# Performance work log

Measured on AMD Instinct MI355X. Metric: run time of the kernel, lower is better.

Reference implementation:

```python
import jax, jax.numpy as jnp
import numpy as np

INTERVAL = 8
HEADS = 4
DIM = 64


def grid_shuffle(x, I):
    # rearrange 'b c (h i) (w j) -> (b i j) c h w' : stride-I residue grouping
    B, C, H, W = x.shape
    h, w = H // I, W // I
    x = x.reshape(B, C, h, I, w, I).transpose(0, 3, 5, 1, 2, 4)
    return x.reshape(B * I * I, C, h, w)


def grid_unshuffle(x, I, B):
    Bp, C, h, w = x.shape
    x = x.reshape(B, I, I, C, h, w).transpose(0, 3, 4, 1, 5, 2)
    return x.reshape(B, C, h * I, w * I)


def conv1x1(x, w, b):
    return jnp.einsum('oc,bchw->bohw', w, x) + b[None, :, None, None]


def pos_bias(h, w, W1, b1, W2, b2):
    # dynamic RPE: MLP over normalized relative coordinates -> [heads, N, N]
    ch = jnp.arange(h)
    cw = jnp.arange(w)
    coords = jnp.stack(jnp.meshgrid(ch, cw, indexing='ij'), -1).reshape(-1, 2).astype(jnp.float32)
    denom = jnp.array([max(h - 1, 1), max(w - 1, 1)], dtype=jnp.float32)
    rel = (coords[:, None, :] - coords[None, :, :]) / denom  # [N,N,2]
    hid = jax.nn.relu(rel @ W1 + b1)
    bias = hid @ W2 + b2  # [N,N,heads]
    return bias.transpose(2, 0, 1)


def mask_attn(q2d, k2d, v2d, bias, pw, pb, heads, scale):
    Bp, C, h, w = q2d.shape
    N, d = h * w, C // heads

    def to_tok(t):  # [Bp,C,h,w] -> [Bp,heads,N,d]
        return t.reshape(Bp, heads, d, N).transpose(0, 1, 3, 2)

    q, k, v = to_tok(q2d), to_tok(k2d), to_tok(v2d)
    attn = jnp.einsum('bhnd,bhmd->bhnm', q * scale, k) + bias[None]
    attn = jax.nn.softmax(attn, axis=-1)
    out = jnp.einsum('bhnm,bhmd->bhnd', attn, v)
    out2d = out.transpose(0, 1, 3, 2).reshape(Bp, C, h, w)
    return conv1x1(out2d, pw, pb)


def setup_inputs() -> dict:
    key = jax.random.key(0)
    ks = jax.random.split(key, 14)
    pos_hidden = DIM // 4  # 16
    s = 0.02
    return {
        'x': jax.random.normal(ks[0], (2, DIM, 160, 160), jnp.float32),
        'qkv_w': jax.random.normal(ks[1], (3 * DIM, DIM), jnp.float32) * s,
        'qkv_b': jnp.zeros((3 * DIM,), jnp.float32),
        'grid_w': jax.random.normal(ks[2], (DIM, DIM), jnp.float32) * s,
        'grid_b': jnp.zeros((DIM,), jnp.float32),
        'pos_w1': jax.random.normal(ks[3], (2, pos_hidden), jnp.float32) * s,
        'pos_b1': jnp.zeros((pos_hidden,), jnp.float32),
        'pos_w2': jax.random.normal(ks[4], (pos_hidden, HEADS), jnp.float32) * s,
        'pos_b2': jnp.zeros((HEADS,), jnp.float32),
        'proj1_w': jax.random.normal(ks[5], (DIM, DIM), jnp.float32) * s,
        'proj1_b': jnp.zeros((DIM,), jnp.float32),
        'proj2_w': jax.random.normal(ks[6], (DIM, DIM), jnp.float32) * s,
        'proj2_b': jnp.zeros((DIM,), jnp.float32),
    }


def reference(x, qkv_w, qkv_b, grid_w, grid_b, pos_w1, pos_b1, pos_w2, pos_b2,
              proj1_w, proj1_b, proj2_w, proj2_b):
    I = INTERVAL
    scale = (DIM // HEADS) ** -0.5
    B, C, H, W = x.shape
    qkv = conv1x1(x, qkv_w, qkv_b)
    x_grid = conv1x1(grid_shuffle(x, I), grid_w, grid_b)
    qkv = grid_shuffle(qkv, I)
    bias = pos_bias(H // I, W // I, pos_w1, pos_b1, pos_w2, pos_b2)
    q, k, v = jnp.split(qkv, 3, axis=1)
    out = mask_attn(x_grid, k, v, bias, proj1_w, proj1_b, HEADS, scale)
    out = mask_attn(q, x_grid, out, bias, proj2_w, proj2_b, HEADS, scale)
    return grid_unshuffle(out, I, B)
```

## Files before the change

kernel.cpp:

```cpp
#include <hip/hip_runtime.h>
#include <hip/hip_bf16.h>


#define N_TOK 400
#define NP    416
#define BP    128

typedef short bf16x8 __attribute__((ext_vector_type(8)));
typedef float f32x16 __attribute__((ext_vector_type(16)));

__device__ inline ushort f2bf(float f) {
    __hip_bfloat16 h = __float2bfloat16(f);
    return *reinterpret_cast<ushort*>(&h);
}
__device__ inline float bf2f(ushort u) {
    union { uint i; float f; } v; v.i = (uint)u << 16; return v.f;
}
__device__ inline uint pk2(float a, float b) {
    return (uint)f2bf(a) | ((uint)f2bf(b) << 16);
}
__device__ inline bf16x8 ld16(const ushort* p) {
    union { uint4 q; bf16x8 v; } u;
    u.q = *reinterpret_cast<const uint4*>(p);
    return u.v;
}
__device__ inline float fast_exp2(float x) {
#if __has_builtin(__builtin_amdgcn_exp2f)
    return __builtin_amdgcn_exp2f(x);
#else
    return __expf(x * 0.6931471805599453f);
#endif
}
__device__ inline float fast_rcp(float x) {
#if __has_builtin(__builtin_amdgcn_rcpf)
    return __builtin_amdgcn_rcpf(x);
#else
    return 1.0f / x;
#endif
}

#define L2E 1.4426950408889634f
#define QK_PRESCALE 0.36067376022224085f

__global__ __launch_bounds__(256) void k_prep(
    const float* __restrict__ W1, const float* __restrict__ B1,
    const float* __restrict__ W2, const float* __restrict__ B2,
    const float* __restrict__ qkv_w, const float* __restrict__ qkv_b,
    const float* __restrict__ grid_w, const float* __restrict__ grid_b,
    const float* __restrict__ p1w, const float* __restrict__ p2w,
    float* __restrict__ biasF, ushort* __restrict__ Wc, float* __restrict__ Bc,
    ushort* __restrict__ Wp1, ushort* __restrict__ Wp2)
{
    int blk = blockIdx.x;
    if (blk < 2704) {
        int idx = blk * 256 + threadIdx.x;
        if (idx >= 692224) return;
        int r = idx & 15, lane = (idx >> 4) & 63;
        int tile = idx >> 10;
        int mt = tile % 13, rem = tile / 13, qt = rem % 13, h = rem / 13;
        int n = qt * 32 + (lane & 31);
        int m = mt * 32 + (r & 3) + 8 * (r >> 2) + 4 * (lane >> 5);
        float val = 0.0f;
        if (n < 400 && m < 400) {
            float r0 = (float)(n / 20 - m / 20) * (1.0f / 19.0f);
            float r1 = (float)(n % 20 - m % 20) * (1.0f / 19.0f);
            float o = B2[h];
#pragma unroll
            for (int k = 0; k < 16; ++k) {
                float hh = r0 * W1[k] + r1 * W1[16 + k] + B1[k];
                hh = fmaxf(hh, 0.0f);
                o += hh * W2[k * 4 + h];
            }
            val = o * L2E;
        }
        biasF[idx] = val;
    } else {
        int t = (blk - 2704) * 256 + threadIdx.x;
        if (t < 16384) {
            int oc = t >> 6, k = t & 63;
            float v = (oc < 192) ? qkv_w[oc * 64 + k] : grid_w[(oc - 192) * 64 + k];
            Wc[t] = f2bf(v);
        } else if (t < 16384 + 4096) {
            Wp1[t - 16384] = f2bf(p1w[t - 16384]);
        } else if (t < 16384 + 8192) {
            Wp2[t - 16384 - 4096] = f2bf(p2w[t - 16384 - 4096]);
        } else if (t < 16384 + 8192 + 256) {
            int oc = t - 16384 - 8192;
            Bc[oc] = (oc < 192) ? qkv_b[oc] : grid_b[oc - 192];
        }
    }
}

__global__ __launch_bounds__(256) void k_conv(
    const float* __restrict__ x, const ushort* __restrict__ Wc,
    const float* __restrict__ Bc,
    ushort* __restrict__ Qb, ushort* __restrict__ Kb,
    ushort* __restrict__ Vb, ushort* __restrict__ XGb)
{
    __shared__ __align__(16) ushort XL[32 * 64];
    int blk = blockIdx.x;
    int b = blk / 800, rem = blk % 800;
    int H0 = rem / 5, wt = rem % 5;
    int w0 = wt * 32;
    int tid = threadIdx.x;

    {
        int c = tid >> 2, q4 = tid & 3;
        const float* xr = x + ((size_t)(b * 64 + c) * 160 + H0) * 160 + w0 + q4 * 8;
        float4 f0 = *reinterpret_cast<const float4*>(xr);
        float4 f1 = *reinterpret_cast<const float4*>(xr + 4);
        char* base = reinterpret_cast<char*>(XL);
#pragma unroll
        for (int k = 0; k < 8; ++k) {
            float v = (k < 4) ? ((const float*)&f0)[k] : ((const float*)&f1)[k - 4];
            int p = q4 * 8 + k;
            int byt = p * 128 + ((2 * c) ^ ((p & 7) << 4));
            *reinterpret_cast<ushort*>(base + byt) = f2bf(v);
        }
    }

    int lane = tid & 63, w = tid >> 6;
    int l31 = lane & 31, hi = lane >> 5;

    bf16x8 wf[2][4];
#pragma unroll
    for (int nt = 0; nt < 2; ++nt)
#pragma unroll
        for (int kk = 0; kk < 4; ++kk)
            wf[nt][kk] = ld16(&Wc[(size_t)(w * 64 + nt * 32 + l31) * 64 + kk * 16 + hi * 8]);
    __syncthreads();

    f32x16 acc0 = 0.0f, acc1 = 0.0f;
    const char* base = reinterpret_cast<const char*>(XL);
#pragma unroll
    for (int kk = 0; kk < 4; ++kk) {
        int byt = l31 * 128 + (((kk * 32 + hi * 16)) ^ ((l31 & 7) << 4));
        bf16x8 xf;
        {
            union { uint4 q; bf16x8 v; } u;
            u.q = *reinterpret_cast<const uint4*>(base + byt);
            xf = u.v;
        }
        acc0 = __builtin_amdgcn_mfma_f32_32x32x16_bf16(wf[0][kk], xf, acc0, 0, 0, 0);
        acc1 = __builtin_amdgcn_mfma_f32_32x32x16_bf16(wf[1][kk], xf, acc1, 0, 0, 0);
    }

    int W0 = w0 + l31, ww = W0 >> 3, j = W0 & 7;
    int bp = b * 64 + (H0 & 7) * 8 + j;
    int n  = (H0 >> 3) * 20 + ww;
    ushort* outb = (w == 0) ? Qb : (w == 1) ? Kb : (w == 2) ? Vb : XGb;
    float mul = (w <= 1) ? QK_PRESCALE : 1.0f;
    ushort* dst = outb + ((size_t)bp * NP + n) * 64;
#pragma unroll
    for (int nt = 0; nt < 2; ++nt) {
        const f32x16& a = nt ? acc1 : acc0;
#pragma unroll
        for (int g = 0; g < 4; ++g) {
            int cc = nt * 32 + 8 * g + 4 * hi;
            int oc = w * 64 + cc;
            uint2 uu;
            uu.x = pk2((a[4 * g + 0] + Bc[oc + 0]) * mul, (a[4 * g + 1] + Bc[oc + 1]) * mul);
            uu.y = pk2((a[4 * g + 2] + Bc[oc + 2]) * mul, (a[4 * g + 3] + Bc[oc + 3]) * mul);
            *reinterpret_cast<uint2*>(dst + cc) = uu;
        }
    }
}

__global__ __launch_bounds__(512, 4) void k_attn_mfma(
    const ushort* __restrict__ Qg, const ushort* __restrict__ Kg,
    const ushort* __restrict__ Vg, const float* __restrict__ biasF,
    ushort* __restrict__ O)
{
    __shared__ ushort Ks[NP * 16];
    __shared__ ushort Vt[16 * 424];
    int blk = blockIdx.x;
    int bp = blk >> 2, h = blk & 3;
    int tid = threadIdx.x;

    const ushort* Ksrc = Kg + (size_t)bp * NP * 64 + h * 16;
#pragma unroll
    for (int it = 0; it < 2; ++it) {
        int i = tid + it * 512;
        if (i < NP * 2) {
            int row = i >> 1, half = i & 1;
            *reinterpret_cast<uint4*>(&Ks[row * 16 + half * 8]) =
                *reinterpret_cast<const uint4*>(&Ksrc[(size_t)row * 64 + half * 8]);
        }
    }
    const ushort* Vsrc = Vg + (size_t)bp * NP * 64 + h * 16;
#pragma unroll
    for (int it = 0; it < 2; ++it) {
        int i = tid + it * 512;
        if (i < 800) {
            int row = i >> 1, hf = i & 1;
            uint4 v = *reinterpret_cast<const uint4*>(&Vsrc[(size_t)row * 64 + hf * 8]);
            const ushort* pv = reinterpret_cast<const ushort*>(&v);
#pragma unroll
            for (int k = 0; k < 8; ++k)
                Vt[(hf * 8 + k) * 424 + row] = pv[k];
        }
    }
    __syncthreads();

    int lane = tid & 63, w = tid >> 6;
    int l31 = lane & 31, hi = lane >> 5;

    for (int qt = w; qt < 13; qt += 8) {
        int qbase = qt * 32;
        bf16x8 qf = ld16(&Qg[((size_t)bp * NP + qbase + l31) * 64 + h * 16 + hi * 8]);
        f32x16 acc = 0.0f;
        const float* bfr = biasF + ((size_t)(h * 169 + qt * 13)) * 1024 + lane * 16;

        float4 cb0 = *reinterpret_cast<const float4*>(bfr + 0);
        float4 cb1 = *reinterpret_cast<const float4*>(bfr + 4);
        float4 cb2 = *reinterpret_cast<const float4*>(bfr + 8);
        float4 cb3 = *reinterpret_cast<const float4*>(bfr + 12);

#pragma unroll
        for (int mt = 0; mt < 13; ++mt) {
            const int mbase = mt * 32;
            float4 nb0, nb1, nb2, nb3;
            if (mt < 12) {
                const float4* nx = reinterpret_cast<const float4*>(bfr + (size_t)(mt + 1) * 1024);
                nb0 = nx[0]; nb1 = nx[1]; nb2 = nx[2]; nb3 = nx[3];
            }

            bf16x8 kf = ld16(&Ks[(mbase + l31) * 16 + hi * 8]);
            f32x16 cin;
            cin[0] = cb0.x; cin[1] = cb0.y; cin[2]  = cb0.z; cin[3]  = cb0.w;
            cin[4] = cb1.x; cin[5] = cb1.y; cin[6]  = cb1.z; cin[7]  = cb1.w;
            cin[8] = cb2.x; cin[9] = cb2.y; cin[10] = cb2.z; cin[11] = cb2.w;
            cin[12] = cb3.x; cin[13] = cb3.y; cin[14] = cb3.z; cin[15] = cb3.w;
            f32x16 sv = __builtin_amdgcn_mfma_f32_32x32x16_bf16(kf, qf, cin, 0, 0, 0);

            const int nv = (mt == 12) ? 8 : 16;
            float p[16];
#pragma unroll
            for (int r = 0; r < 16; ++r)
                if (r < nv) p[r] = fast_exp2(sv[r]);

            {
                uint c4 = pk2(p[0], p[1]), c5 = pk2(p[2], p[3]);
                uint c6 = pk2(p[4], p[5]), c7 = pk2(p[6], p[7]);
                asm("v_permlane32_swap_b32 %0, %1" : "+v"(c4), "+v"(c6));
                asm("v_permlane32_swap_b32 %0, %1" : "+v"(c5), "+v"(c7));
                union { uint u[4]; bf16x8 v; } A;
                A.u[0] = c4; A.u[1] = c5; A.u[2] = c6; A.u[3] = c7;
                bf16x8 vf;
                if (l31 < 16) vf = ld16(&Vt[l31 * 424 + mbase + hi * 8]);
                else { union { uint u[4]; bf16x8 v; } o; o.u[0]=o.u[1]=o.u[2]=o.u[3]=0x3F803F80u; vf = o.v; }
                acc = __builtin_amdgcn_mfma_f32_32x32x16_bf16(A.v, vf, acc, 0, 0, 0);
            }
            if (mt < 12) {
                uint c4 = pk2(p[8], p[9]),  c5 = pk2(p[10], p[11]);
                uint c6 = pk2(p[12], p[13]), c7 = pk2(p[14], p[15]);
                asm("v_permlane32_swap_b32 %0, %1" : "+v"(c4), "+v"(c6));
                asm("v_permlane32_swap_b32 %0, %1" : "+v"(c5), "+v"(c7));
                union { uint u[4]; bf16x8 v; } A;
                A.u[0] = c4; A.u[1] = c5; A.u[2] = c6; A.u[3] = c7;
                bf16x8 vf;
                if (l31 < 16) vf = ld16(&Vt[l31 * 424 + mbase + 16 + hi * 8]);
                else { union { uint u[4]; bf16x8 v; } o; o.u[0]=o.u[1]=o.u[2]=o.u[3]=0x3F803F80u; vf = o.v; }
                acc = __builtin_amdgcn_mfma_f32_32x32x16_bf16(A.v, vf, acc, 0, 0, 0);
            }
            cb0 = nb0; cb1 = nb1; cb2 = nb2; cb3 = nb3;
        }

#pragma unroll
        for (int r = 0; r < 16; ++r) {
            int moff = (r & 3) + 8 * (r >> 2) + 4 * hi;
            int q = qbase + moff;
            float s = __shfl(acc[r], lane | 16);
            if (l31 < 16 && q < N_TOK)
                O[((size_t)bp * 400 + q) * 64 + h * 16 + l31] = f2bf(acc[r] * fast_rcp(s));
        }
    }
}

template<int MODE>
__global__ __launch_bounds__(256) void k_proj(
    const ushort* __restrict__ In, const ushort* __restrict__ Wp,
    const float* __restrict__ Bv, ushort* __restrict__ Out)
{
    __shared__ __align__(16) ushort XL[128 * 64];
    size_t t0 = (size_t)blockIdx.x * 128;
    int tid = threadIdx.x;

    char* basec = reinterpret_cast<char*>(XL);
#pragma unroll
    for (int it = 0; it < 4; ++it) {
        int idx = tid + it * 256;
        int p = idx >> 3, c8 = idx & 7;
        uint4 v = *reinterpret_cast<const uint4*>(In + (t0 + p) * 64 + c8 * 8);
        int byt = p * 128 + ((c8 * 16) ^ ((p & 7) << 4));
        *reinterpret_cast<uint4*>(basec + byt) = v;
    }

    int lane = tid & 63, w = tid >> 6;
    int l31 = lane & 31, hi = lane >> 5;

    bf16x8 wf[2][4];
#pragma unroll
    for (int nt = 0; nt < 2; ++nt)
#pragma unroll
        for (int kk = 0; kk < 4; ++kk)
            wf[nt][kk] = ld16(&Wp[(size_t)(nt * 32 + l31) * 64 + kk * 16 + hi * 8]);
    __syncthreads();

    int prow = w * 32 + l31;
    f32x16 acc0 = 0.0f, acc1 = 0.0f;
#pragma unroll
    for (int kk = 0; kk < 4; ++kk) {
        int byt = prow * 128 + (((kk * 32 + hi * 16)) ^ ((prow & 7) << 4));
        union { uint4 q; bf16x8 v; } u;
        u.q = *reinterpret_cast<const uint4*>(basec + byt);
        acc0 = __builtin_amdgcn_mfma_f32_32x32x16_bf16(wf[0][kk], u.v, acc0, 0, 0, 0);
        acc1 = __builtin_amdgcn_mfma_f32_32x32x16_bf16(wf[1][kk], u.v, acc1, 0, 0, 0);
    }

    size_t t = t0 + prow;
    ushort* dst;
    if (MODE == 0) {
        int bp = (int)(t / 400), n = (int)(t % 400);
        dst = Out + ((size_t)bp * NP + n) * 64;
    } else {
        dst = Out + t * 64;
    }
#pragma unroll
    for (int nt = 0; nt < 2; ++nt) {
        const f32x16& a = nt ? acc1 : acc0;
#pragma unroll
        for (int g = 0; g < 4; ++g) {
            int cc = nt * 32 + 8 * g + 4 * hi;
            uint2 uu;
            uu.x = pk2(a[4 * g + 0] + Bv[cc + 0], a[4 * g + 1] + Bv[cc + 1]);
            uu.y = pk2(a[4 * g + 2] + Bv[cc + 2], a[4 * g + 3] + Bv[cc + 3]);
            *reinterpret_cast<uint2*>(dst + cc) = uu;
        }
    }
}

__global__ __launch_bounds__(256) void k_unshuffle(
    const ushort* __restrict__ In, float* __restrict__ out)
{
    __shared__ __align__(16) ushort il[160 * 64];
    int blk = blockIdx.x;
    int b = blk / 160, rem = blk % 160, iI = rem / 20, hh = rem % 20;
    int tid = threadIdx.x;

    for (int idx = tid; idx < 1280; idx += 256) {
        int j = idx / 160, r2 = idx % 160, ww = r2 / 8, c8 = r2 % 8;
        int bp = b * 64 + iI * 8 + j;
        int n  = hh * 20 + ww;
        uint4 v = reinterpret_cast<const uint4*>(In + ((size_t)bp * 400 + n) * 64)[c8];
        reinterpret_cast<uint4*>(&il[(ww * 8 + j) * 64])[c8] = v;
    }
    __syncthreads();

    int c = tid >> 2, q = tid & 3;
    int H0 = hh * 8 + iI;
    float* og = out + ((size_t)(b * 64 + c) * 160 + H0) * 160;
#pragma unroll
    for (int k = 0; k < 10; ++k) {
        int f = q + 4 * k;
        float4 v;
        v.x = bf2f(il[(4 * f + 0) * 64 + c]);
        v.y = bf2f(il[(4 * f + 1) * 64 + c]);
        v.z = bf2f(il[(4 * f + 2) * 64 + c]);
        v.w = bf2f(il[(4 * f + 3) * 64 + c]);
        reinterpret_cast<float4*>(og)[f] = v;
    }
}

extern "C" void kernel_launch(void* const* d_in, const int* in_sizes, int n_in,
                              void* d_out, int out_size, void* d_ws, size_t ws_size,
                              hipStream_t stream)
{
    const float* x      = (const float*)d_in[0];
    const float* qkv_w  = (const float*)d_in[1];
    const float* qkv_b  = (const float*)d_in[2];
    const float* grid_w = (const float*)d_in[3];
    const float* grid_b = (const float*)d_in[4];
    const float* pw1    = (const float*)d_in[5];
    const float* pb1    = (const float*)d_in[6];
    const float* pw2    = (const float*)d_in[7];
    const float* pb2    = (const float*)d_in[8];
    const float* p1w    = (const float*)d_in[9];
    const float* p1b    = (const float*)d_in[10];
    const float* p2w    = (const float*)d_in[11];
    const float* p2b    = (const float*)d_in[12];

    char* W = (char*)d_ws;
    float*  biasF = (float*)(W + 0);
    ushort* Wc    = (ushort*)(W + 2768896);
    ushort* Wp1   = (ushort*)(W + 2801664);
    ushort* Wp2   = (ushort*)(W + 2809856);
    float*  Bc    = (float*) (W + 2818048);
    const size_t BASE2 = 2819072;
    const size_t BB = (size_t)BP * NP * 64 * 2;
    ushort* Qb = (ushort*)(W + BASE2);
    ushort* Kb = (ushort*)(W + BASE2 + 1 * BB);
    ushort* Vb = (ushort*)(W + BASE2 + 2 * BB);
    ushort* XG = (ushort*)(W + BASE2 + 3 * BB);
    ushort* P1 = (ushort*)(W + BASE2 + 4 * BB);
    const size_t OB = (size_t)BP * 400 * 64 * 2;
    ushort* O1 = (ushort*)(W + BASE2 + 5 * BB);
    ushort* O2 = (ushort*)(W + BASE2 + 5 * BB + OB);
    ushort* OFb = O1;
    float*  out = (float*)d_out;

    k_prep<<<2801, 256, 0, stream>>>(pw1, pb1, pw2, pb2, qkv_w, qkv_b, grid_w, grid_b,
                                     p1w, p2w, biasF, Wc, Bc, Wp1, Wp2);
    k_conv<<<1600, 256, 0, stream>>>(x, Wc, Bc, Qb, Kb, Vb, XG);
    k_attn_mfma<<<512, 512, 0, stream>>>(XG, Kb, Vb, biasF, O1);
    k_proj<0><<<400, 256, 0, stream>>>(O1, Wp1, p1b, P1);
    k_attn_mfma<<<512, 512, 0, stream>>>(Qb, XG, P1, biasF, O2);
    k_proj<1><<<400, 256, 0, stream>>>(O2, Wp2, p2b, OFb);
    k_unshuffle<<<320, 256, 0, stream>>>(OFb, out);
}
```

Measured before the change: 116.0 us.

## Split attention query tiles across two blocks per head for balanced waves

Each (batch, head) attention block is split into two blocks handling 7 and 6 query tiles, so every wave processes at most one tile instead of some waves doing two. The grid doubles to 1024 blocks and unused waves exit early. This removes the per-block tail where a few waves do double work, at the cost of loading K and V into shared memory twice per head. The bias load is also simplified to a single 16-float vector load.

```diff
diff --git a/kernel.cpp b/kernel.cpp
--- a/kernel.cpp
+++ b/kernel.cpp
@@ -174,7 +174,9 @@
     __shared__ ushort Ks[NP * 16];
     __shared__ ushort Vt[16 * 424];
     int blk = blockIdx.x;
-    int bp = blk >> 2, h = blk & 3;
+    int bp = blk >> 3, h = (blk >> 1) & 3, sub = blk & 1;
+    int qt0 = sub ? 7 : 0;
+    int cnt = sub ? 6 : 7;
     int tid = threadIdx.x;
 
     const ushort* Ksrc = Kg + (size_t)bp * NP * 64 + h * 16;
@@ -205,75 +207,65 @@
     int lane = tid & 63, w = tid >> 6;
     int l31 = lane & 31, hi = lane >> 5;
 
-    for (int qt = w; qt < 13; qt += 8) {
-        int qbase = qt * 32;
-        bf16x8 qf = ld16(&Qg[((size_t)bp * NP + qbase + l31) * 64 + h * 16 + hi * 8]);
-        f32x16 acc = 0.0f;
-        const float* bfr = biasF + ((size_t)(h * 169 + qt * 13)) * 1024 + lane * 16;
-
-        float4 cb0 = *reinterpret_cast<const float4*>(bfr + 0);
-        float4 cb1 = *reinterpret_cast<const float4*>(bfr + 4);
-        float4 cb2 = *reinterpret_cast<const float4*>(bfr + 8);
-        float4 cb3 = *reinterpret_cast<const float4*>(bfr + 12);
-
-#pragma unroll
-        for (int mt = 0; mt < 13; ++mt) {
-            const int mbase = mt * 32;
-            float4 nb0, nb1, nb2, nb3;
-            if (mt < 12) {
-                const float4* nx = reinterpret_cast<const float4*>(bfr + (size_t)(mt + 1) * 1024);
-                nb0 = nx[0]; nb1 = nx[1]; nb2 = nx[2]; nb3 = nx[3];
-            }
-
-            bf16x8 kf = ld16(&Ks[(mbase + l31) * 16 + hi * 8]);
-            f32x16 cin;
-            cin[0] = cb0.x; cin[1] = cb0.y; cin[2]  = cb0.z; cin[3]  = cb0.w;
-            cin[4] = cb1.x; cin[5] = cb1.y; cin[6]  = cb1.z; cin[7]  = cb1.w;
-            cin[8] = cb2.x; cin[9] = cb2.y; cin[10] = cb2.z; cin[11] = cb2.w;
-            cin[12] = cb3.x; cin[13] = cb3.y; cin[14] = cb3.z; cin[15] = cb3.w;
-            f32x16 sv = __builtin_amdgcn_mfma_f32_32x32x16_bf16(kf, qf, cin, 0, 0, 0);
-
-            const int nv = (mt == 12) ? 8 : 16;
-            float p[16];
-#pragma unroll
-            for (int r = 0; r < 16; ++r)
-                if (r < nv) p[r] = fast_exp2(sv[r]);
-
-            {
-                uint c4 = pk2(p[0], p[1]), c5 = pk2(p[2], p[3]);
-                uint c6 = pk2(p[4], p[5]), c7 = pk2(p[6], p[7]);
-                asm("v_permlane32_swap_b32 %0, %1" : "+v"(c4), "+v"(c6));
-                asm("v_permlane32_swap_b32 %0, %1" : "+v"(c5), "+v"(c7));
-                union { uint u[4]; bf16x8 v; } A;
-                A.u[0] = c4; A.u[1] = c5; A.u[2] = c6; A.u[3] = c7;
-                bf16x8 vf;
-                if (l31 < 16) vf = ld16(&Vt[l31 * 424 + mbase + hi * 8]);
-                else { union { uint u[4]; bf16x8 v; } o; o.u[0]=o.u[1]=o.u[2]=o.u[3]=0x3F803F80u; vf = o.v; }
-                acc = __builtin_amdgcn_mfma_f32_32x32x16_bf16(A.v, vf, acc, 0, 0, 0);
-            }
-            if (mt < 12) {
-                uint c4 = pk2(p[8], p[9]),  c5 = pk2(p[10], p[11]);
-                uint c6 = pk2(p[12], p[13]), c7 = pk2(p[14], p[15]);
-                asm("v_permlane32_swap_b32 %0, %1" : "+v"(c4), "+v"(c6));
-                asm("v_permlane32_swap_b32 %0, %1" : "+v"(c5), "+v"(c7));
-                union { uint u[4]; bf16x8 v; } A;
-                A.u[0] = c4; A.u[1] = c5; A.u[2] = c6; A.u[3] = c7;
-                bf16x8 vf;
-                if (l31 < 16) vf = ld16(&Vt[l31 * 424 + mbase + 16 + hi * 8]);
-                else { union { uint u[4]; bf16x8 v; } o; o.u[0]=o.u[1]=o.u[2]=o.u[3]=0x3F803F80u; vf = o.v; }
-                acc = __builtin_amdgcn_mfma_f32_32x32x16_bf16(A.v, vf, acc, 0, 0, 0);
-            }
-            cb0 = nb0; cb1 = nb1; cb2 = nb2; cb3 = nb3;
-        }
-
-#pragma unroll
-        for (int r = 0; r < 16; ++r) {
-            int moff = (r & 3) + 8 * (r >> 2) + 4 * hi;
-            int q = qbase + moff;
-            float s = __shfl(acc[r], lane | 16);
-            if (l31 < 16 && q < N_TOK)
-                O[((size_t)bp * 400 + q) * 64 + h * 16 + l31] = f2bf(acc[r] * fast_rcp(s));
-        }
+    if (w >= cnt) return;
+    int qt = qt0 + w;
+    int qbase = qt * 32;
+    bf16x8 qf = ld16(&Qg[((size_t)bp * NP + qbase + l31) * 64 + h * 16 + hi * 8]);
+    f32x16 acc = 0.0f;
+    const f32x16* bfr = reinterpret_cast<const f32x16*>(
+        biasF + ((size_t)(h * 169 + qt * 13)) * 1024 + lane * 16);
+
+    f32x16 cb = bfr[0];
+
+#pragma unroll
+    for (int mt = 0; mt < 13; ++mt) {
+        const int mbase = mt * 32;
+        f32x16 nb;
+        if (mt < 12) nb = bfr[mt + 1];
+
+        bf16x8 kf = ld16(&Ks[(mbase + l31) * 16 + hi * 8]);
+        f32x16 sv = __builtin_amdgcn_mfma_f32_32x32x16_bf16(kf, qf, cb, 0, 0, 0);
+
+        const int nv = (mt == 12) ? 8 : 16;
+        float p[16];
+#pragma unroll
+        for (int r = 0; r < 16; ++r)
+            if (r < nv) p[r] = fast_exp2(sv[r]);
+
+        {
+            uint c4 = pk2(p[0], p[1]), c5 = pk2(p[2], p[3]);
+            uint c6 = pk2(p[4], p[5]), c7 = pk2(p[6], p[7]);
+            asm("v_permlane32_swap_b32 %0, %1" : "+v"(c4), "+v"(c6));
+            asm("v_permlane32_swap_b32 %0, %1" : "+v"(c5), "+v"(c7));
+            union { uint u[4]; bf16x8 v; } A;
+            A.u[0] = c4; A.u[1] = c5; A.u[2] = c6; A.u[3] = c7;
+            bf16x8 vf;
+            if (l31 < 16) vf = ld16(&Vt[l31 * 424 + mbase + hi * 8]);
+            else { union { uint u[4]; bf16x8 v; } o; o.u[0]=o.u[1]=o.u[2]=o.u[3]=0x3F803F80u; vf = o.v; }
+            acc = __builtin_amdgcn_mfma_f32_32x32x16_bf16(A.v, vf, acc, 0, 0, 0);
+        }
+        if (mt < 12) {
+            uint c4 = pk2(p[8], p[9]),  c5 = pk2(p[10], p[11]);
+            uint c6 = pk2(p[12], p[13]), c7 = pk2(p[14], p[15]);
+            asm("v_permlane32_swap_b32 %0, %1" : "+v"(c4), "+v"(c6));
+            asm("v_permlane32_swap_b32 %0, %1" : "+v"(c5), "+v"(c7));
+            union { uint u[4]; bf16x8 v; } A;
+            A.u[0] = c4; A.u[1] = c5; A.u[2] = c6; A.u[3] = c7;
+            bf16x8 vf;
+            if (l31 < 16) vf = ld16(&Vt[l31 * 424 + mbase + 16 + hi * 8]);
+            else { union { uint u[4]; bf16x8 v; } o; o.u[0]=o.u[1]=o.u[2]=o.u[3]=0x3F803F80u; vf = o.v; }
+            acc = __builtin_amdgcn_mfma_f32_32x32x16_bf16(A.v, vf, acc, 0, 0, 0);
+        }
+        cb = nb;
+    }
+
+#pragma unroll
+    for (int r = 0; r < 16; ++r) {
+        int moff = (r & 3) + 8 * (r >> 2) + 4 * hi;
+        int q = qbase + moff;
+        float s = __shfl(acc[r], lane | 16);
+        if (l31 < 16 && q < N_TOK)
+            O[((size_t)bp * 400 + q) * 64 + h * 16 + l31] = f2bf(acc[r] * fast_rcp(s));
     }
 }
 
@@ -412,9 +404,9 @@
     k_prep<<<2801, 256, 0, stream>>>(pw1, pb1, pw2, pb2, qkv_w, qkv_b, grid_w, grid_b,
                                      p1w, p2w, biasF, Wc, Bc, Wp1, Wp2);
     k_conv<<<1600, 256, 0, stream>>>(x, Wc, Bc, Qb, Kb, Vb, XG);
-    k_attn_mfma<<<512, 512, 0, stream>>>(XG, Kb, Vb, biasF, O1);
+    k_attn_mfma<<<1024, 512, 0, stream>>>(XG, Kb, Vb, biasF, O1);
     k_proj<0><<<400, 256, 0, stream>>>(O1, Wp1, p1b, P1);
-    k_attn_mfma<<<512, 512, 0, stream>>>(Qb, XG, P1, biasF, O2);
+    k_attn_mfma<<<1024, 512, 0, stream>>>(Qb, XG, P1, biasF, O2);
     k_proj<1><<<400, 256, 0, stream>>>(O2, Wp2, p2b, OFb);
     k_unshuffle<<<320, 256, 0, stream>>>(OFb, out);
 }
```

Result: slower. 127.2 us (+9.6%).
